# Optimization experiments

Measured on AMD Instinct MI355X. Metric: run time of the kernel, lower is better.

## Reference

```python
import jax, jax.numpy as jnp
import numpy as np

MAX_DEPTH = 8
LMBDA = 0.1
OUTPUT_DIM = 128


def setup_inputs() -> dict:
    key = jax.random.key(0)
    k1, k2, k3, k4, k5, k6 = jax.random.split(key, 6)
    B, D, C = 8192, 2048, OUTPUT_DIM
    n_inner = 2 ** MAX_DEPTH - 1  # 255 inner nodes, BFS order
    n_leaf = 2 ** MAX_DEPTH       # 256 leaves
    x = jax.random.normal(k1, (B, D), dtype=jnp.float32)
    target = jax.random.randint(k2, (B,), 0, C)
    # small scale so sigmoid gates are not saturated (log(pen), log(1-pen) finite)
    W = jax.random.normal(k3, (n_inner, D), dtype=jnp.float32) * 0.02
    b = jax.random.normal(k4, (n_inner,), dtype=jnp.float32) * 0.02
    beta = jax.random.normal(k5, (n_inner,), dtype=jnp.float32)
    leaf_params = jax.random.normal(k6, (n_leaf, C), dtype=jnp.float32)
    return {"x": x, "target": target, "W": W, "b": b, "beta": beta,
            "leaf_params": leaf_params}


def reference(x, target, W, b, beta, leaf_params):
    B = x.shape[0]
    C = leaf_params.shape[1]
    y = jax.nn.one_hot(target, C, dtype=x.dtype)  # target_onehot

    # All inner-node gates as one batched GEMM: p[b,i] = sigmoid(beta_i*(x@w_i+b_i))
    p = jax.nn.sigmoid(beta[None, :] * (x @ W.T + b[None, :]))  # [B, n_inner]

    # Level-by-level path probability propagation (BFS node order).
    path = jnp.ones((B, 1), x.dtype)
    penalties = []  # per-level [2^d] node penalties
    start = 0
    for d in range(MAX_DEPTH):
        n = 2 ** d
        p_lvl = p[:, start:start + n]                      # [B, 2^d]
        pen = jnp.sum(p_lvl * path, axis=0) / jnp.sum(path, axis=0)
        penalties.append(pen)
        # left child gets path*(1-p), right gets path*p; interleave -> next level
        path = jnp.stack([path * (1.0 - p_lvl), path * p_lvl], axis=-1).reshape(B, 2 * n)
        start += n
    # path: [B, n_leaf] leaf path probabilities (left-to-right order)

    Q = jax.nn.softmax(leaf_params, axis=-1)               # [n_leaf, C]
    TQ = y @ jnp.log(Q).T                                  # [B, n_leaf], y . log Q per leaf
    loss = jnp.mean(jnp.sum(path * TQ, axis=1))

    # Penalty C: only inner nodes whose children are NOT leaves contribute
    # (original get_penalty drops depth==max_depth nodes), depths 1..max_depth-1.
    Cpen = jnp.asarray(0.0, x.dtype)
    for d in range(MAX_DEPTH - 1):
        lam = LMBDA * 2.0 ** (-(d + 1))
        pen = penalties[d]
        Cpen = Cpen - lam * 0.5 * jnp.sum(jnp.log(pen) + jnp.log(1.0 - pen))

    total = -loss + Cpen

    # output: Q of the max-path-prob leaf per sample
    leaf_idx = jnp.argmax(path, axis=1)                    # [B]
    output = Q[leaf_idx]                                   # [B, C]
    return total, output
```

## Files before the change

### kernel.cpp

```cpp
#include <hip/hip_runtime.h>
#include <hip/hip_bf16.h>
#include <hip/hip_fp16.h>
#include <stdint.h>

#define B_SIZE 8192
#define D_SIZE 2048
#define C_SIZE 128
#define N_INNER 255
#define N_LEAF 256
#define NPAD 256
#define NBLK_PATH 512

typedef _Float16 half8 __attribute__((ext_vector_type(8)));
typedef __fp16 pk16x2 __attribute__((ext_vector_type(2)));
typedef float f32x4 __attribute__((ext_vector_type(4)));
typedef unsigned short u16;

__device__ unsigned int g_path_done = 0;

__device__ inline uint32_t pkh(float a, float b) {
    pk16x2 h = __builtin_amdgcn_cvt_pkrtz(a, b);
    return __builtin_bit_cast(uint32_t, h);
}
__device__ inline void split4(const float4 v, uint2& hi, uint2& lo) {
    pk16x2 a01 = __builtin_amdgcn_cvt_pkrtz(v.x, v.y);
    pk16x2 a23 = __builtin_amdgcn_cvt_pkrtz(v.z, v.w);
    float r0 = v.x - (float)a01[0];
    float r1 = v.y - (float)a01[1];
    float r2 = v.z - (float)a23[0];
    float r3 = v.w - (float)a23[1];
    hi = make_uint2(__builtin_bit_cast(uint32_t, a01), __builtin_bit_cast(uint32_t, a23));
    lo = make_uint2(pkh(r0, r1), pkh(r2, r3));
}

__global__ __launch_bounds__(256) void prep_kernel(
    const float* __restrict__ Wsrc, u16* __restrict__ Wh, u16* __restrict__ Wl,
    const float* __restrict__ lp, float* __restrict__ Q, float* __restrict__ logQt,
    float* __restrict__ gacc)
{
    int bid = blockIdx.x;
    int t = threadIdx.x;
    if (bid < 256) {
        int row = bid;
        int k = t * 8;
        uint2 h0, l0, h1, l1;
        if (row < N_INNER) {
            float4 v0 = *(const float4*)(Wsrc + (size_t)row * D_SIZE + k);
            float4 v1 = *(const float4*)(Wsrc + (size_t)row * D_SIZE + k + 4);
            split4(v0, h0, l0); split4(v1, h1, l1);
        } else {
            h0 = l0 = h1 = l1 = make_uint2(0u, 0u);
        }
        *(uint2*)&Wh[(size_t)row * D_SIZE + k]     = h0;
        *(uint2*)&Wh[(size_t)row * D_SIZE + k + 4] = h1;
        *(uint2*)&Wl[(size_t)row * D_SIZE + k]     = l0;
        *(uint2*)&Wl[(size_t)row * D_SIZE + k + 4] = l1;
    } else {
        int row = bid - 256;
        if (bid == 256) gacc[t] = 0.f;
        __shared__ float red[128];
        float v = 0.f;
        if (t < 128) { v = lp[row * C_SIZE + t]; red[t] = v; }
        __syncthreads();
        for (int s = 64; s > 0; s >>= 1) { if (t < s) red[t] = fmaxf(red[t], red[t + s]); __syncthreads(); }
        float mx = red[0]; __syncthreads();
        float e = 0.f;
        if (t < 128) { e = expf(v - mx); red[t] = e; }
        __syncthreads();
        for (int s = 64; s > 0; s >>= 1) { if (t < s) red[t] += red[t + s]; __syncthreads(); }
        float sum = red[0];
        if (t < 128) {
            Q[row * C_SIZE + t] = e / sum;
            logQt[(size_t)t * N_LEAF + row] = (v - mx) - logf(sum);
        }
    }
}

#define GBM 64
#define GBK 32
#define GKSPLIT 4
#define KCHUNK (D_SIZE / GKSPLIT)
#define KITERS (KCHUNK / GBK)
#define LDKA 40

__global__ __launch_bounds__(256, 2) void gemm_mfma(
    const float* __restrict__ x, const u16* __restrict__ Wh, const u16* __restrict__ Wl,
    float* __restrict__ zp)
{
    __shared__ __align__(16) u16 sAh[4][GBM * LDKA];
    __shared__ __align__(16) u16 sAl[4][GBM * LDKA];

    const int t = threadIdx.x;
    const int lane = t & 63, w = t >> 6;
    const int lr = lane & 15, lq = lane >> 4;
    const int mi = blockIdx.x >> 2;
    const int kz = blockIdx.x & 3;
    const int m0 = mi * GBM;
    const int kb0 = kz * KCHUNK;

    f32x4 acc[4][4];
    #pragma unroll
    for (int mt = 0; mt < 4; ++mt)
        #pragma unroll
        for (int nt = 0; nt < 4; ++nt) acc[mt][nt] = (f32x4){0.f, 0.f, 0.f, 0.f};

    float4 av_c[8];
    #pragma unroll
    for (int i = 0; i < 8; ++i) {
        int idx = i * 64 + lane;
        int row = idx >> 3, ch = idx & 7;
        av_c[i] = *(const float4*)(x + (size_t)(m0 + row) * D_SIZE + kb0 + ch * 4);
    }
    half8 bh[4], bl[4];
    #pragma unroll
    for (int nt = 0; nt < 4; ++nt) {
        int row = w * 64 + nt * 16 + lr;
        bh[nt] = *(const half8*)(Wh + (size_t)row * D_SIZE + kb0 + lq * 8);
        bl[nt] = *(const half8*)(Wl + (size_t)row * D_SIZE + kb0 + lq * 8);
    }

    #pragma unroll
    for (int kt = 0; kt < KITERS; ++kt) {
        const int kb = kb0 + kt * GBK;
        half8 nbh[4], nbl[4];
        if (kt + 1 < KITERS) {
            #pragma unroll
            for (int nt = 0; nt < 4; ++nt) {
                int row = w * 64 + nt * 16 + lr;
                nbh[nt] = *(const half8*)(Wh + (size_t)row * D_SIZE + kb + GBK + lq * 8);
                nbl[nt] = *(const half8*)(Wl + (size_t)row * D_SIZE + kb + GBK + lq * 8);
            }
        }
        float4 av_n[8];
        if (kt + 1 < KITERS) {
            #pragma unroll
            for (int i = 0; i < 8; ++i) {
                int idx = i * 64 + lane;
                int row = idx >> 3, ch = idx & 7;
                av_n[i] = *(const float4*)(x + (size_t)(m0 + row) * D_SIZE + kb + GBK + ch * 4);
            }
        }
        #pragma unroll
        for (int i = 0; i < 8; ++i) {
            int idx = i * 64 + lane;
            int row = idx >> 3, ch = idx & 7;
            uint2 hi, lo; split4(av_c[i], hi, lo);
            *(uint2*)&sAh[w][row * LDKA + ch * 4] = hi;
            *(uint2*)&sAl[w][row * LDKA + ch * 4] = lo;
        }
        asm volatile("s_waitcnt lgkmcnt(0)" ::: "memory");
        half8 ah[4], al[4];
        #pragma unroll
        for (int mt = 0; mt < 4; ++mt) {
            int off = (mt * 16 + lr) * LDKA + lq * 8;
            ah[mt] = *(const half8*)&sAh[w][off];
            al[mt] = *(const half8*)&sAl[w][off];
        }
        #pragma unroll
        for (int mt = 0; mt < 4; ++mt)
            #pragma unroll
            for (int nt = 0; nt < 4; ++nt) {
                acc[mt][nt] = __builtin_amdgcn_mfma_f32_16x16x32_f16(ah[mt], bh[nt], acc[mt][nt], 0, 0, 0);
                acc[mt][nt] = __builtin_amdgcn_mfma_f32_16x16x32_f16(ah[mt], bl[nt], acc[mt][nt], 0, 0, 0);
                acc[mt][nt] = __builtin_amdgcn_mfma_f32_16x16x32_f16(al[mt], bh[nt], acc[mt][nt], 0, 0, 0);
            }
        if (kt + 1 < KITERS) {
            #pragma unroll
            for (int i = 0; i < 8; ++i) av_c[i] = av_n[i];
            #pragma unroll
            for (int nt = 0; nt < 4; ++nt) { bh[nt] = nbh[nt]; bl[nt] = nbl[nt]; }
        }
    }

    float* zout = zp + (size_t)kz * B_SIZE * NPAD;
    #pragma unroll
    for (int mt = 0; mt < 4; ++mt) {
        #pragma unroll
        for (int nt = 0; nt < 4; ++nt) {
            int gn = w * 64 + nt * 16 + lr;
            #pragma unroll
            for (int r = 0; r < 4; ++r) {
                int gm = m0 + mt * 16 + lq * 4 + r;
                zout[(size_t)gm * NPAD + gn] = acc[mt][nt][r];
            }
        }
    }
}

__global__ __launch_bounds__(256) void path_kernel(
    const float* __restrict__ z, const int* __restrict__ target,
    const float* __restrict__ bvec, const float* __restrict__ beta,
    const float* __restrict__ Q, const float* __restrict__ logQt,
    float* __restrict__ gacc, float* __restrict__ out)
{
    __shared__ float pbuf[4][256];
    __shared__ float s_num[128], s_den[128], s_loss;
    __shared__ int s_last;
    const int t = threadIdx.x, w = t >> 6, lane = t & 63;
    const int c0 = lane * 4;
    float pnum[4] = {0.f, 0.f, 0.f, 0.f};
    float pden[4] = {0.f, 0.f, 0.f, 0.f};
    float loss = 0.f;

    if (t < 128) s_num[t] = 0.f;
    else s_den[t - 128] = 0.f;
    if (t == 0) s_loss = 0.f;
    __syncthreads();

    float bet[4], bia[4];
    #pragma unroll
    for (int j = 0; j < 4; ++j) {
        int c = c0 + j;
        bet[j] = (c < N_INNER) ? beta[c] : 0.f;
        bia[j] = (c < N_INNER) ? bvec[c] : 0.f;
    }

    for (int i = 0; i < 4; ++i) {
        int r = blockIdx.x * 16 + w * 4 + i;
        float4 s = make_float4(0.f, 0.f, 0.f, 0.f);
        #pragma unroll
        for (int p = 0; p < GKSPLIT; ++p) {
            float4 v = *(const float4*)(z + ((size_t)p * B_SIZE + r) * NPAD + c0);
            s.x += v.x; s.y += v.y; s.z += v.z; s.w += v.w;
        }
        float zv[4] = {s.x, s.y, s.z, s.w};
        float pv[4];
        #pragma unroll
        for (int j = 0; j < 4; ++j) {
            int c = c0 + j;
            pv[j] = (c < N_INNER) ? 1.f / (1.f + expf(-bet[j] * (zv[j] + bia[j]))) : 0.f;
        }
        *(float4*)&pbuf[w][c0] = make_float4(pv[0], pv[1], pv[2], pv[3]);
        asm volatile("s_waitcnt lgkmcnt(0)" ::: "memory");

        int tg = target[r];
        float4 lq4 = *(const float4*)(logQt + (size_t)tg * N_LEAF + c0);
        float lqa[4] = {lq4.x, lq4.y, lq4.z, lq4.w};

        float P = 1.f;
        #pragma unroll
        for (int d = 0; d < 6; ++d) {
            int node = (1 << d) - 1 + (c0 >> (8 - d));
            int bit = (c0 >> (7 - d)) & 1;
            float pvn = pbuf[w][node];
            P *= bit ? pvn : (1.f - pvn);
        }
        float p6  = pbuf[w][63 + lane];
        float p7a = pbuf[w][127 + 2 * lane];
        float p7b = pbuf[w][127 + 2 * lane + 1];
        float lsum = 0.f, bestV = -1.f;
        int bestI = 0;
        #pragma unroll
        for (int j = 0; j < 4; ++j) {
            float t6 = (j & 2) ? p6 : (1.f - p6);
            float p7 = (j & 2) ? p7b : p7a;
            float t7 = (j & 1) ? p7 : (1.f - p7);
            float pl = (P * t6) * t7;
            lsum += pl * lqa[j];
            if (pl > bestV) { bestV = pl; bestI = c0 + j; }
        }
        if (lane < 32) {
            #pragma unroll
            for (int j = 0; j < 4; ++j) {
                int c = c0 + j;
                if (c < 127) {
                    int h = c + 1; int d = 31 - __clz(h);
                    float pp = 1.f;
                    for (int e = 0; e < d; ++e) {
                        int ha = h >> (d - e);
                        int bit = (h >> (d - 1 - e)) & 1;
                        float pvn = pbuf[w][ha - 1];
                        pp *= bit ? pvn : (1.f - pvn);
                    }
                    pnum[j] += pbuf[w][c] * pp;
                    pden[j] += pp;
                }
            }
        }
        #pragma unroll
        for (int m = 1; m < 64; m <<= 1) {
            lsum += __shfl_xor(lsum, m, 64);
            float ov = __shfl_xor(bestV, m, 64);
            int   oi = __shfl_xor(bestI, m, 64);
            if (ov > bestV || (ov == bestV && oi < bestI)) { bestV = ov; bestI = oi; }
        }
        loss += lsum;
        out[1 + (size_t)r * C_SIZE + lane]      = Q[bestI * C_SIZE + lane];
        out[1 + (size_t)r * C_SIZE + lane + 64] = Q[bestI * C_SIZE + lane + 64];
        asm volatile("" ::: "memory");
    }

    if (lane < 32) {
        #pragma unroll
        for (int j = 0; j < 4; ++j) {
            int c = c0 + j;
            if (c < 127) {
                atomicAdd(&s_num[c], pnum[j]);
                atomicAdd(&s_den[c], pden[j]);
            }
        }
    }
    if (lane == 0) atomicAdd(&s_loss, loss);
    __syncthreads();
    if (t < 127)        atomicAdd(&gacc[t], s_num[t]);
    else if (t == 127)  atomicAdd(&gacc[127], s_loss);
    else if (t < 255)   atomicAdd(&gacc[t], s_den[t - 128]);

    __threadfence();
    if (t == 0) {
        unsigned int prev = atomicAdd(&g_path_done, 1u);
        s_last = (prev == NBLK_PATH - 1) ? 1 : 0;
    }
    __syncthreads();
    if (s_last) {
        __shared__ float fs[256];
        __shared__ float fred[128];
        float v = 0.f;
        if (t < 255) v = atomicAdd(&gacc[t], 0.f);
        fs[t] = v;
        __syncthreads();
        float term = 0.f;
        if (t < 127) {
            int d = 31 - __clz(t + 1);
            float lam = 0.1f * exp2f(-(float)(d + 1));
            float pen = fs[t] / fs[128 + t];
            term = lam * 0.5f * (logf(pen) + logf(1.f - pen));
        }
        if (t < 128) { fred[t] = term; }
        __syncthreads();
        for (int sh = 64; sh > 0; sh >>= 1) { if (t < sh) fred[t] += fred[t + sh]; __syncthreads(); }
        if (t == 0) {
            out[0] = -(fs[127] / (float)B_SIZE) - fred[0];
            atomicExch(&g_path_done, 0u);
        }
    }
}

extern "C" void kernel_launch(void* const* d_in, const int* in_sizes, int n_in,
                              void* d_out, int out_size, void* d_ws, size_t ws_size,
                              hipStream_t stream)
{
    const float* x    = (const float*)d_in[0];
    const int*   tgt  = (const int*)d_in[1];
    const float* W    = (const float*)d_in[2];
    const float* b    = (const float*)d_in[3];
    const float* beta = (const float*)d_in[4];
    const float* lp   = (const float*)d_in[5];
    float* out = (float*)d_out;

    float* z     = (float*)d_ws;
    float* Q     = z + (size_t)GKSPLIT * B_SIZE * NPAD;
    float* logQt = Q + (size_t)N_LEAF * C_SIZE;
    u16*   Wh    = (u16*)(logQt + (size_t)C_SIZE * N_LEAF);
    u16*   Wl    = Wh + (size_t)N_LEAF * D_SIZE;
    float* gacc  = (float*)(Wl + (size_t)N_LEAF * D_SIZE);

    prep_kernel<<<512, 256, 0, stream>>>(W, Wh, Wl, lp, Q, logQt, gacc);

    gemm_mfma<<<512, 256, 0, stream>>>(x, Wh, Wl, z);

    path_kernel<<<NBLK_PATH, 256, 0, stream>>>(
        z, tgt, b, beta, Q, logQt, gacc, out);
}
```

Baseline: 201.2 us.

## Process one row per wave in path kernel and split finalize into separate launch

The path kernel now handles one sample row per wavefront, using 2048 blocks instead of looping over four rows per wave in 512 blocks, which exposes more parallelism to hide memory latency. The last-block-done counter with threadfence and atomic readback is removed, and the final penalty/loss reduction moves into a separate single-block finalize kernel. In exchange, global atomics on gacc rise fourfold and one extra kernel launch is added.

```diff
diff --git a/kernel.cpp b/kernel.cpp
--- a/kernel.cpp
+++ b/kernel.cpp
@@ -9,14 +9,12 @@
 #define N_INNER 255
 #define N_LEAF 256
 #define NPAD 256
-#define NBLK_PATH 512
+#define NBLK_PATH 2048
 
 typedef _Float16 half8 __attribute__((ext_vector_type(8)));
 typedef __fp16 pk16x2 __attribute__((ext_vector_type(2)));
 typedef float f32x4 __attribute__((ext_vector_type(4)));
 typedef unsigned short u16;
-
-__device__ unsigned int g_path_done = 0;
 
 __device__ inline uint32_t pkh(float a, float b) {
     pk16x2 h = __builtin_amdgcn_cvt_pkrtz(a, b);
@@ -195,18 +193,16 @@
 {
     __shared__ float pbuf[4][256];
     __shared__ float s_num[128], s_den[128], s_loss;
-    __shared__ int s_last;
     const int t = threadIdx.x, w = t >> 6, lane = t & 63;
     const int c0 = lane * 4;
-    float pnum[4] = {0.f, 0.f, 0.f, 0.f};
-    float pden[4] = {0.f, 0.f, 0.f, 0.f};
-    float loss = 0.f;
 
     if (t < 128) s_num[t] = 0.f;
     else s_den[t - 128] = 0.f;
     if (t == 0) s_loss = 0.f;
     __syncthreads();
 
+    const int r = blockIdx.x * 4 + w;
+
     float bet[4], bia[4];
     #pragma unroll
     for (int j = 0; j < 4; ++j) {
@@ -215,80 +211,79 @@
         bia[j] = (c < N_INNER) ? bvec[c] : 0.f;
     }
 
-    for (int i = 0; i < 4; ++i) {
-        int r = blockIdx.x * 16 + w * 4 + i;
-        float4 s = make_float4(0.f, 0.f, 0.f, 0.f);
-        #pragma unroll
-        for (int p = 0; p < GKSPLIT; ++p) {
-            float4 v = *(const float4*)(z + ((size_t)p * B_SIZE + r) * NPAD + c0);
-            s.x += v.x; s.y += v.y; s.z += v.z; s.w += v.w;
-        }
-        float zv[4] = {s.x, s.y, s.z, s.w};
-        float pv[4];
+    float4 s = make_float4(0.f, 0.f, 0.f, 0.f);
+    #pragma unroll
+    for (int p = 0; p < GKSPLIT; ++p) {
+        float4 v = *(const float4*)(z + ((size_t)p * B_SIZE + r) * NPAD + c0);
+        s.x += v.x; s.y += v.y; s.z += v.z; s.w += v.w;
+    }
+    float zv[4] = {s.x, s.y, s.z, s.w};
+    float pv[4];
+    #pragma unroll
+    for (int j = 0; j < 4; ++j) {
+        int c = c0 + j;
+        pv[j] = (c < N_INNER) ? 1.f / (1.f + expf(-bet[j] * (zv[j] + bia[j]))) : 0.f;
+    }
+    *(float4*)&pbuf[w][c0] = make_float4(pv[0], pv[1], pv[2], pv[3]);
+    asm volatile("s_waitcnt lgkmcnt(0)" ::: "memory");
+
+    int tg = target[r];
+    float4 lq4 = *(const float4*)(logQt + (size_t)tg * N_LEAF + c0);
+    float lqa[4] = {lq4.x, lq4.y, lq4.z, lq4.w};
+
+    float P = 1.f;
+    #pragma unroll
+    for (int d = 0; d < 6; ++d) {
+        int node = (1 << d) - 1 + (c0 >> (8 - d));
+        int bit = (c0 >> (7 - d)) & 1;
+        float pvn = pbuf[w][node];
+        P *= bit ? pvn : (1.f - pvn);
+    }
+    float p6  = pbuf[w][63 + lane];
+    float p7a = pbuf[w][127 + 2 * lane];
+    float p7b = pbuf[w][127 + 2 * lane + 1];
+    float lsum = 0.f, bestV = -1.f;
+    int bestI = 0;
+    #pragma unroll
+    for (int j = 0; j < 4; ++j) {
+        float t6 = (j & 2) ? p6 : (1.f - p6);
+        float p7 = (j & 2) ? p7b : p7a;
+        float t7 = (j & 1) ? p7 : (1.f - p7);
+        float pl = (P * t6) * t7;
+        lsum += pl * lqa[j];
+        if (pl > bestV) { bestV = pl; bestI = c0 + j; }
+    }
+
+    float pnum[4] = {0.f, 0.f, 0.f, 0.f};
+    float pden[4] = {0.f, 0.f, 0.f, 0.f};
+    if (lane < 32) {
         #pragma unroll
         for (int j = 0; j < 4; ++j) {
             int c = c0 + j;
-            pv[j] = (c < N_INNER) ? 1.f / (1.f + expf(-bet[j] * (zv[j] + bia[j]))) : 0.f;
-        }
-        *(float4*)&pbuf[w][c0] = make_float4(pv[0], pv[1], pv[2], pv[3]);
-        asm volatile("s_waitcnt lgkmcnt(0)" ::: "memory");
-
-        int tg = target[r];
-        float4 lq4 = *(const float4*)(logQt + (size_t)tg * N_LEAF + c0);
-        float lqa[4] = {lq4.x, lq4.y, lq4.z, lq4.w};
-
-        float P = 1.f;
-        #pragma unroll
-        for (int d = 0; d < 6; ++d) {
-            int node = (1 << d) - 1 + (c0 >> (8 - d));
-            int bit = (c0 >> (7 - d)) & 1;
-            float pvn = pbuf[w][node];
-            P *= bit ? pvn : (1.f - pvn);
-        }
-        float p6  = pbuf[w][63 + lane];
-        float p7a = pbuf[w][127 + 2 * lane];
-        float p7b = pbuf[w][127 + 2 * lane + 1];
-        float lsum = 0.f, bestV = -1.f;
-        int bestI = 0;
-        #pragma unroll
-        for (int j = 0; j < 4; ++j) {
-            float t6 = (j & 2) ? p6 : (1.f - p6);
-            float p7 = (j & 2) ? p7b : p7a;
-            float t7 = (j & 1) ? p7 : (1.f - p7);
-            float pl = (P * t6) * t7;
-            lsum += pl * lqa[j];
-            if (pl > bestV) { bestV = pl; bestI = c0 + j; }
-        }
-        if (lane < 32) {
-            #pragma unroll
-            for (int j = 0; j < 4; ++j) {
-                int c = c0 + j;
-                if (c < 127) {
-                    int h = c + 1; int d = 31 - __clz(h);
-                    float pp = 1.f;
-                    for (int e = 0; e < d; ++e) {
-                        int ha = h >> (d - e);
-                        int bit = (h >> (d - 1 - e)) & 1;
-                        float pvn = pbuf[w][ha - 1];
-                        pp *= bit ? pvn : (1.f - pvn);
-                    }
-                    pnum[j] += pbuf[w][c] * pp;
-                    pden[j] += pp;
+            if (c < 127) {
+                int h = c + 1; int d = 31 - __clz(h);
+                float pp = 1.f;
+                for (int e = 0; e < d; ++e) {
+                    int ha = h >> (d - e);
+                    int bit = (h >> (d - 1 - e)) & 1;
+                    float pvn = pbuf[w][ha - 1];
+                    pp *= bit ? pvn : (1.f - pvn);
                 }
-            }
-        }
-        #pragma unroll
-        for (int m = 1; m < 64; m <<= 1) {
-            lsum += __shfl_xor(lsum, m, 64);
-            float ov = __shfl_xor(bestV, m, 64);
-            int   oi = __shfl_xor(bestI, m, 64);
-            if (ov > bestV || (ov == bestV && oi < bestI)) { bestV = ov; bestI = oi; }
-        }
-        loss += lsum;
-        out[1 + (size_t)r * C_SIZE + lane]      = Q[bestI * C_SIZE + lane];
-        out[1 + (size_t)r * C_SIZE + lane + 64] = Q[bestI * C_SIZE + lane + 64];
-        asm volatile("" ::: "memory");
-    }
+                pnum[j] = pbuf[w][c] * pp;
+                pden[j] = pp;
+            }
+        }
+    }
+
+    #pragma unroll
+    for (int m = 1; m < 64; m <<= 1) {
+        lsum += __shfl_xor(lsum, m, 64);
+        float ov = __shfl_xor(bestV, m, 64);
+        int   oi = __shfl_xor(bestI, m, 64);
+        if (ov > bestV || (ov == bestV && oi < bestI)) { bestV = ov; bestI = oi; }
+    }
+    out[1 + (size_t)r * C_SIZE + lane]      = Q[bestI * C_SIZE + lane];
+    out[1 + (size_t)r * C_SIZE + lane + 64] = Q[bestI * C_SIZE + lane + 64];
 
     if (lane < 32) {
         #pragma unroll
@@ -300,40 +295,32 @@
             }
         }
     }
-    if (lane == 0) atomicAdd(&s_loss, loss);
+    if (lane == 0) atomicAdd(&s_loss, lsum);
     __syncthreads();
     if (t < 127)        atomicAdd(&gacc[t], s_num[t]);
     else if (t == 127)  atomicAdd(&gacc[127], s_loss);
     else if (t < 255)   atomicAdd(&gacc[t], s_den[t - 128]);
-
-    __threadfence();
-    if (t == 0) {
-        unsigned int prev = atomicAdd(&g_path_done, 1u);
-        s_last = (prev == NBLK_PATH - 1) ? 1 : 0;
-    }
+}
+
+__global__ __launch_bounds__(256) void finalize_kernel(
+    const float* __restrict__ gacc, float* __restrict__ out)
+{
+    __shared__ float fs[256];
+    __shared__ float fred[128];
+    int t = threadIdx.x;
+    fs[t] = (t < 255) ? gacc[t] : 0.f;
     __syncthreads();
-    if (s_last) {
-        __shared__ float fs[256];
-        __shared__ float fred[128];
-        float v = 0.f;
-        if (t < 255) v = atomicAdd(&gacc[t], 0.f);
-        fs[t] = v;
-        __syncthreads();
-        float term = 0.f;
-        if (t < 127) {
-            int d = 31 - __clz(t + 1);
-            float lam = 0.1f * exp2f(-(float)(d + 1));
-            float pen = fs[t] / fs[128 + t];
-            term = lam * 0.5f * (logf(pen) + logf(1.f - pen));
-        }
-        if (t < 128) { fred[t] = term; }
-        __syncthreads();
-        for (int sh = 64; sh > 0; sh >>= 1) { if (t < sh) fred[t] += fred[t + sh]; __syncthreads(); }
-        if (t == 0) {
-            out[0] = -(fs[127] / (float)B_SIZE) - fred[0];
-            atomicExch(&g_path_done, 0u);
-        }
-    }
+    float term = 0.f;
+    if (t < 127) {
+        int d = 31 - __clz(t + 1);
+        float lam = 0.1f * exp2f(-(float)(d + 1));
+        float pen = fs[t] / fs[128 + t];
+        term = lam * 0.5f * (logf(pen) + logf(1.f - pen));
+    }
+    if (t < 128) { fred[t] = term; }
+    __syncthreads();
+    for (int sh = 64; sh > 0; sh >>= 1) { if (t < sh) fred[t] += fred[t + sh]; __syncthreads(); }
+    if (t == 0) out[0] = -(fs[127] / (float)B_SIZE) - fred[0];
 }
 
 extern "C" void kernel_launch(void* const* d_in, const int* in_sizes, int n_in,
@@ -361,4 +348,6 @@
 
     path_kernel<<<NBLK_PATH, 256, 0, stream>>>(
         z, tgt, b, beta, Q, logQt, gacc, out);
-}
+
+    finalize_kernel<<<1, 256, 0, stream>>>(gacc, out);
+}
```

Result: slower. 221.4 us (+10.0%).
